# Kernel tuning notes

Measured on AMD Instinct MI355X. Metric: run time of the kernel, lower is better.

## Reference

```python
import jax, jax.numpy as jnp
import numpy as np

N, F, F_, H = 8192, 1024, 64, 4
LEAKY_ALPHA = 0.2
MASK_VAL = -1e10


def setup_inputs() -> dict:
    key = jax.random.key(0)
    k1, k2, k3, k4 = jax.random.split(key, 4)
    X = jax.random.normal(k1, (N, F), dtype=jnp.float32)
    # sparse-ish binary adjacency with self loops (A = A + I in the source script)
    A = (jax.random.uniform(k2, (N, N)) < 0.004).astype(jnp.float32)
    A = jnp.clip(A + jnp.eye(N, dtype=jnp.float32), 0.0, 1.0)
    W = jax.random.normal(k3, (H, F, F_), dtype=jnp.float32) * (1.0 / np.sqrt(F))
    attn_a = jax.random.normal(k4, (H, 2 * F_, 1), dtype=jnp.float32) * (1.0 / np.sqrt(2 * F_))
    bias = jnp.zeros((H, F_), dtype=jnp.float32)
    return {"X": X, "A": A, "W": W, "attn_a": attn_a, "bias": bias}


def reference(X, A, W, attn_a, bias):
    # features per head: [H, N, F_]
    feats = jnp.einsum('nf,hfk->hnk', X, W)
    # concat-score trick: [f_i, f_j] @ a == f_i @ a[:F_] + f_j @ a[F_:]
    a_self = attn_a[:, :F_, 0]   # [H, F_]
    a_neigh = attn_a[:, F_:, 0]  # [H, F_]
    s_self = jnp.einsum('hnk,hk->hn', feats, a_self)   # [H, N]
    s_neigh = jnp.einsum('hnk,hk->hn', feats, a_neigh)  # [H, N]
    scores = s_self[:, :, None] + s_neigh[:, None, :]   # [H, N, N]
    scores = jnp.where(scores > 0, scores, LEAKY_ALPHA * scores)  # LeakyReLU(0.2)
    scores = scores + MASK_VAL * (1.0 - A)[None]
    attn = jax.nn.softmax(scores, axis=-1)              # [H, N, N]
    # aggregate (dropout is identity at inference)
    out = jnp.einsum('hij,hjk->hik', attn, feats) + bias[:, None, :]  # [H, N, F_]
    out = jnp.transpose(out, (1, 0, 2)).reshape(X.shape[0], H * F_)   # concat heads
    return jax.nn.relu(out)
```

## Files before the change

### kernel.cpp

```cpp
#include <hip/hip_runtime.h>
#include <hip/hip_bf16.h>
#include <stdint.h>

#define NN 8192
#define FF 1024
#define FD 64
#define NH 4
#define CC 256
#define MAXE 192

typedef __attribute__((ext_vector_type(8))) short short8;
typedef __attribute__((ext_vector_type(4))) float f32x4;

__device__ __forceinline__ short bf16_rne(float f) {
    union { float f; uint32_t u; } v; v.f = f;
    uint32_t r = (v.u + 0x7FFFu + ((v.u >> 16) & 1u)) >> 16;
    return (short)(r & 0xFFFFu);
}
__device__ __forceinline__ float bf2f(short s) {
    union { uint32_t u; float f; } v; v.u = ((uint32_t)(uint16_t)s) << 16;
    return v.f;
}

__global__ __launch_bounds__(256) void wt_kernel(const float* __restrict__ W,
                                                 short* __restrict__ Wt) {
    int gid = blockIdx.x * 256 + threadIdx.x;
    int k = gid & 1023;
    int n = (gid >> 10) & 63;
    int h = gid >> 16;
    Wt[gid] = bf16_rne(W[(h << 16) + k * 64 + n]);
}

__global__ __launch_bounds__(256) void mega_kernel(const float* __restrict__ X,
                                                   const short* __restrict__ Wt,
                                                   const float* __restrict__ attn_a,
                                                   const float* __restrict__ A,
                                                   short* __restrict__ featb,
                                                   float* __restrict__ s_self4,
                                                   float* __restrict__ s_neigh4,
                                                   int* __restrict__ nbr,
                                                   int* __restrict__ cnt) {
    __shared__ short Xs[64 * 40];
    __shared__ short Ws[64 * 40];
    const int b = blockIdx.x;
    const int t = threadIdx.x;

    if (b < 512) {
        const int h  = b & 3;
        const int m0 = (b >> 2) * 64;
        const int wave = t >> 6, lane = t & 63;
        const int q = lane >> 4, nl = lane & 15;
        const int srow = t >> 2, sk8 = (t & 3) * 8;

        f32x4 acc0 = {0.f,0.f,0.f,0.f}, acc1 = {0.f,0.f,0.f,0.f};
        f32x4 acc2 = {0.f,0.f,0.f,0.f}, acc3 = {0.f,0.f,0.f,0.f};

        const float* Xp = X + (size_t)(m0 + srow) * FF + sk8;
        const short* Wp = Wt + (size_t)(h * 64 + srow) * FF + sk8;

        for (int k0 = 0; k0 < FF; k0 += 32) {
            float4 x0 = *(const float4*)(Xp + k0);
            float4 x1 = *(const float4*)(Xp + k0 + 4);
            short8 wv = *(const short8*)(Wp + k0);
            short8 xv;
            xv[0] = bf16_rne(x0.x); xv[1] = bf16_rne(x0.y);
            xv[2] = bf16_rne(x0.z); xv[3] = bf16_rne(x0.w);
            xv[4] = bf16_rne(x1.x); xv[5] = bf16_rne(x1.y);
            xv[6] = bf16_rne(x1.z); xv[7] = bf16_rne(x1.w);
            *(short8*)(&Xs[srow * 40 + sk8]) = xv;
            *(short8*)(&Ws[srow * 40 + sk8]) = wv;
            __syncthreads();
            short8 a  = *(const short8*)(&Xs[(wave * 16 + nl) * 40 + q * 8]);
            short8 b0 = *(const short8*)(&Ws[( 0 + nl) * 40 + q * 8]);
            short8 b1 = *(const short8*)(&Ws[(16 + nl) * 40 + q * 8]);
            short8 b2 = *(const short8*)(&Ws[(32 + nl) * 40 + q * 8]);
            short8 b3 = *(const short8*)(&Ws[(48 + nl) * 40 + q * 8]);
            acc0 = __builtin_amdgcn_mfma_f32_16x16x32_bf16(a, b0, acc0, 0, 0, 0);
            acc1 = __builtin_amdgcn_mfma_f32_16x16x32_bf16(a, b1, acc1, 0, 0, 0);
            acc2 = __builtin_amdgcn_mfma_f32_16x16x32_bf16(a, b2, acc2, 0, 0, 0);
            acc3 = __builtin_amdgcn_mfma_f32_16x16x32_bf16(a, b3, acc3, 0, 0, 0);
            __syncthreads();
        }
        const int row = m0 + wave * 16 + q * 4;
        const int colbase = h * 64 + nl;
        for (int r = 0; r < 4; ++r) {
            short* fr = featb + (size_t)(row + r) * CC + colbase;
            fr[ 0] = bf16_rne(acc0[r]);
            fr[16] = bf16_rne(acc1[r]);
            fr[32] = bf16_rne(acc2[r]);
            fr[48] = bf16_rne(acc3[r]);
        }
        const float A0 = attn_a[h * 128 + nl],      A1 = attn_a[h * 128 + nl + 16];
        const float A2 = attn_a[h * 128 + nl + 32], A3 = attn_a[h * 128 + nl + 48];
        const float B0 = attn_a[h * 128 + 64 + nl],      B1 = attn_a[h * 128 + 64 + nl + 16];
        const float B2 = attn_a[h * 128 + 64 + nl + 32], B3 = attn_a[h * 128 + 64 + nl + 48];
        for (int r = 0; r < 4; ++r) {
            float ps = acc0[r] * A0 + acc1[r] * A1 + acc2[r] * A2 + acc3[r] * A3;
            float pn = acc0[r] * B0 + acc1[r] * B1 + acc2[r] * B2 + acc3[r] * B3;
            for (int off = 1; off < 16; off <<= 1) {
                ps += __shfl_xor(ps, off);
                pn += __shfl_xor(pn, off);
            }
            if (nl == 0) {
                s_self4 [(row + r) * 4 + h] = ps;
                s_neigh4[(row + r) * 4 + h] = pn;
            }
        }
    } else {
        int* idx = (int*)Xs;
        int* c   = (int*)Ws;
        const int row = b - 512;
        if (t == 0) *c = 0;
        __syncthreads();
        const f32x4* A4 = (const f32x4*)(A + (size_t)row * NN);
        for (int r = 0; r < 8; ++r) {
            int c4 = r * 256 + t;
            f32x4 v = __builtin_nontemporal_load(&A4[c4]);
            if (v.x > 0.5f) { int p = atomicAdd(c, 1); if (p < MAXE) idx[p] = c4 * 4 + 0; }
            if (v.y > 0.5f) { int p = atomicAdd(c, 1); if (p < MAXE) idx[p] = c4 * 4 + 1; }
            if (v.z > 0.5f) { int p = atomicAdd(c, 1); if (p < MAXE) idx[p] = c4 * 4 + 2; }
            if (v.w > 0.5f) { int p = atomicAdd(c, 1); if (p < MAXE) idx[p] = c4 * 4 + 3; }
        }
        __syncthreads();
        int n = min(*c, MAXE);
        if (t < n) nbr[row * MAXE + t] = idx[t];
        if (t == 0) cnt[row] = n;
    }
}

__global__ __launch_bounds__(256) void smax_kernel(const int* __restrict__ nbr,
                                                   const int* __restrict__ cnt,
                                                   const short* __restrict__ featb,
                                                   const float* __restrict__ s_self4,
                                                   const float* __restrict__ s_neigh4,
                                                   const float* __restrict__ bias,
                                                   float* __restrict__ out) {
    __shared__ int js[MAXE];
    __shared__ float scs[NH][MAXE];
    const int row = blockIdx.x;
    const int t = threadIdx.x;
    const int h = t >> 6, lane = t & 63;
    const int n = cnt[row];
    if (t < n) js[t] = nbr[row * MAXE + t];
    __syncthreads();

    const f32x4 ss = *(const f32x4*)(s_self4 + row * 4);
    if (t < n) {
        f32x4 sn = *(const f32x4*)(s_neigh4 + js[t] * 4);
        #pragma unroll
        for (int hh = 0; hh < NH; ++hh) {
            float s = ss[hh] + sn[hh];
            scs[hh][t] = s > 0.f ? s : 0.2f * s;
        }
    }
    __syncthreads();

    float m = -1e30f;
    #pragma unroll
    for (int i = 0; i < 3; ++i) {
        int e = lane + 64 * i;
        if (e < n) m = fmaxf(m, scs[h][e]);
    }
    for (int off = 1; off < 64; off <<= 1) m = fmaxf(m, __shfl_xor(m, off));
    float dsum = 0.f;
    #pragma unroll
    for (int i = 0; i < 3; ++i) {
        int e = lane + 64 * i;
        if (e < n) {
            float p = __expf(scs[h][e] - m);
            scs[h][e] = p;
            dsum += p;
        }
    }
    for (int off = 1; off < 64; off <<= 1) dsum += __shfl_xor(dsum, off);

    const int sub = lane >> 3;
    const int l8  = lane & 7;
    const short* fb = featb + h * 64 + l8 * 8;
    f32x4 accA = {0.f,0.f,0.f,0.f}, accB = {0.f,0.f,0.f,0.f};
    for (int e = sub; e < n; e += 8) {
        int j = js[e];
        float p = scs[h][e];
        short8 f = *(const short8*)(fb + (size_t)j * CC);
        accA[0] = fmaf(p, bf2f(f[0]), accA[0]);
        accA[1] = fmaf(p, bf2f(f[1]), accA[1]);
        accA[2] = fmaf(p, bf2f(f[2]), accA[2]);
        accA[3] = fmaf(p, bf2f(f[3]), accA[3]);
        accB[0] = fmaf(p, bf2f(f[4]), accB[0]);
        accB[1] = fmaf(p, bf2f(f[5]), accB[1]);
        accB[2] = fmaf(p, bf2f(f[6]), accB[2]);
        accB[3] = fmaf(p, bf2f(f[7]), accB[3]);
    }
    #pragma unroll
    for (int k = 0; k < 4; ++k) {
        accA[k] += __shfl_xor(accA[k], 8);
        accA[k] += __shfl_xor(accA[k], 16);
        accA[k] += __shfl_xor(accA[k], 32);
        accB[k] += __shfl_xor(accB[k], 8);
        accB[k] += __shfl_xor(accB[k], 16);
        accB[k] += __shfl_xor(accB[k], 32);
    }
    if (sub == 0) {
        float rd = 1.0f / dsum;
        const float* bp = bias + h * 64 + l8 * 8;
        f32x4 oA, oB;
        #pragma unroll
        for (int k = 0; k < 4; ++k) {
            oA[k] = fmaxf(accA[k] * rd + bp[k],     0.f);
            oB[k] = fmaxf(accB[k] * rd + bp[k + 4], 0.f);
        }
        float* op = out + (size_t)row * CC + h * 64 + l8 * 8;
        *(f32x4*)op       = oA;
        *(f32x4*)(op + 4) = oB;
    }
}

extern "C" void kernel_launch(void* const* d_in, const int* in_sizes, int n_in,
                              void* d_out, int out_size, void* d_ws, size_t ws_size,
                              hipStream_t stream) {
    const float* X      = (const float*)d_in[0];
    const float* A      = (const float*)d_in[1];
    const float* W      = (const float*)d_in[2];
    const float* attn_a = (const float*)d_in[3];
    const float* bias   = (const float*)d_in[4];
    float* out = (float*)d_out;

    char* ws = (char*)d_ws;
    short* featb    = (short*)ws;
    float* s_self4  = (float*)(ws + 4194304);
    float* s_neigh4 = (float*)(ws + 4325376);
    short* Wt       = (short*)(ws + 4456448);
    int*   nbr      = (int*)  (ws + 4980736);
    int*   cnt      = (int*)  (ws + 11272192);

    wt_kernel  <<<1024, 256, 0, stream>>>(W, Wt);
    mega_kernel<<<512 + NN, 256, 0, stream>>>(X, Wt, attn_a, A,
                                              featb, s_self4, s_neigh4, nbr, cnt);
    smax_kernel<<<NN, 256, 0, stream>>>(nbr, cnt, featb, s_self4, s_neigh4, bias, out);
}
```

Baseline: 406.6 us.

## Fuse all stages into one cooperative persistent kernel with grid syncs

Merges the W transpose, the adjacency compaction, the feature GEMM and the sparse softmax aggregation into a single cooperative kernel of 1024 persistent blocks, separated by grid-wide syncs. It is meant to remove the launch overhead and tail gaps between three kernels. In exchange, the GEMM phase now runs on only 512 of the 1024 blocks while the rest sit idle, the A-scan no longer overlaps with the GEMM, and the grid syncs add cost. The design also depends on all 1024 blocks being co-resident.

New measurement: 694.0 us. 1.71x slower.

```diff
diff --git a/kernel.cpp b/kernel.cpp
--- a/kernel.cpp
+++ b/kernel.cpp
@@ -1,13 +1,15 @@
 #include <hip/hip_runtime.h>
-#include <hip/hip_bf16.h>
+#include <hip/hip_cooperative_groups.h>
 #include <stdint.h>
+
+namespace cg = cooperative_groups;
 
 #define NN 8192
 #define FF 1024
-#define FD 64
 #define NH 4
 #define CC 256
 #define MAXE 192
+#define GRID 1024
 
 typedef __attribute__((ext_vector_type(8))) short short8;
 typedef __attribute__((ext_vector_type(4))) float f32x4;
@@ -22,30 +24,55 @@
     return v.f;
 }
 
-__global__ __launch_bounds__(256) void wt_kernel(const float* __restrict__ W,
-                                                 short* __restrict__ Wt) {
-    int gid = blockIdx.x * 256 + threadIdx.x;
-    int k = gid & 1023;
-    int n = (gid >> 10) & 63;
-    int h = gid >> 16;
-    Wt[gid] = bf16_rne(W[(h << 16) + k * 64 + n]);
-}
-
-__global__ __launch_bounds__(256) void mega_kernel(const float* __restrict__ X,
-                                                   const short* __restrict__ Wt,
-                                                   const float* __restrict__ attn_a,
-                                                   const float* __restrict__ A,
-                                                   short* __restrict__ featb,
-                                                   float* __restrict__ s_self4,
-                                                   float* __restrict__ s_neigh4,
-                                                   int* __restrict__ nbr,
-                                                   int* __restrict__ cnt) {
-    __shared__ short Xs[64 * 40];
-    __shared__ short Ws[64 * 40];
+__global__ __launch_bounds__(256, 4) void fused_kernel(
+    const float* __restrict__ X, const float* __restrict__ A,
+    const float* __restrict__ W, const float* __restrict__ attn_a,
+    const float* __restrict__ bias,
+    short* __restrict__ Wt, short* __restrict__ featb,
+    float* __restrict__ s_self4, float* __restrict__ s_neigh4,
+    int* __restrict__ nbr, int* __restrict__ cnt,
+    float* __restrict__ out)
+{
+    cg::grid_group grid = cg::this_grid();
+    __shared__ short lds[2 * 64 * 40];
+    __shared__ int c;
     const int b = blockIdx.x;
     const int t = threadIdx.x;
 
+    {
+        int gid = b * 256 + t;
+        int k = gid & 1023, n = (gid >> 10) & 63, h = gid >> 16;
+        Wt[gid] = bf16_rne(W[(h << 16) + k * 64 + n]);
+    }
+
+    {
+        int* idx = (int*)lds;
+        for (int row = b; row < NN; row += GRID) {
+            if (t == 0) c = 0;
+            __syncthreads();
+            const f32x4* A4 = (const f32x4*)(A + (size_t)row * NN);
+            #pragma unroll
+            for (int r = 0; r < 8; ++r) {
+                int c4 = r * 256 + t;
+                f32x4 v = __builtin_nontemporal_load(&A4[c4]);
+                if (v.x > 0.5f) { int p = atomicAdd(&c, 1); if (p < MAXE) idx[p] = c4 * 4 + 0; }
+                if (v.y > 0.5f) { int p = atomicAdd(&c, 1); if (p < MAXE) idx[p] = c4 * 4 + 1; }
+                if (v.z > 0.5f) { int p = atomicAdd(&c, 1); if (p < MAXE) idx[p] = c4 * 4 + 2; }
+                if (v.w > 0.5f) { int p = atomicAdd(&c, 1); if (p < MAXE) idx[p] = c4 * 4 + 3; }
+            }
+            __syncthreads();
+            int n = min(c, MAXE);
+            if (t < n) nbr[row * MAXE + t] = idx[t];
+            if (t == 0) cnt[row] = n;
+            __syncthreads();
+        }
+    }
+
+    grid.sync();
+
     if (b < 512) {
+        short* Xs = lds;
+        short* Ws = lds + 64 * 40;
         const int h  = b & 3;
         const int m0 = (b >> 2) * 64;
         const int wave = t >> 6, lane = t & 63;
@@ -106,112 +133,92 @@
                 s_neigh4[(row + r) * 4 + h] = pn;
             }
         }
-    } else {
-        int* idx = (int*)Xs;
-        int* c   = (int*)Ws;
-        const int row = b - 512;
-        if (t == 0) *c = 0;
-        __syncthreads();
-        const f32x4* A4 = (const f32x4*)(A + (size_t)row * NN);
-        for (int r = 0; r < 8; ++r) {
-            int c4 = r * 256 + t;
-            f32x4 v = __builtin_nontemporal_load(&A4[c4]);
-            if (v.x > 0.5f) { int p = atomicAdd(c, 1); if (p < MAXE) idx[p] = c4 * 4 + 0; }
-            if (v.y > 0.5f) { int p = atomicAdd(c, 1); if (p < MAXE) idx[p] = c4 * 4 + 1; }
-            if (v.z > 0.5f) { int p = atomicAdd(c, 1); if (p < MAXE) idx[p] = c4 * 4 + 2; }
-            if (v.w > 0.5f) { int p = atomicAdd(c, 1); if (p < MAXE) idx[p] = c4 * 4 + 3; }
-        }
-        __syncthreads();
-        int n = min(*c, MAXE);
-        if (t < n) nbr[row * MAXE + t] = idx[t];
-        if (t == 0) cnt[row] = n;
-    }
-}
-
-__global__ __launch_bounds__(256) void smax_kernel(const int* __restrict__ nbr,
-                                                   const int* __restrict__ cnt,
-                                                   const short* __restrict__ featb,
-                                                   const float* __restrict__ s_self4,
-                                                   const float* __restrict__ s_neigh4,
-                                                   const float* __restrict__ bias,
-                                                   float* __restrict__ out) {
-    __shared__ int js[MAXE];
-    __shared__ float scs[NH][MAXE];
-    const int row = blockIdx.x;
-    const int t = threadIdx.x;
-    const int h = t >> 6, lane = t & 63;
-    const int n = cnt[row];
-    if (t < n) js[t] = nbr[row * MAXE + t];
-    __syncthreads();
-
-    const f32x4 ss = *(const f32x4*)(s_self4 + row * 4);
-    if (t < n) {
-        f32x4 sn = *(const f32x4*)(s_neigh4 + js[t] * 4);
-        #pragma unroll
-        for (int hh = 0; hh < NH; ++hh) {
-            float s = ss[hh] + sn[hh];
-            scs[hh][t] = s > 0.f ? s : 0.2f * s;
-        }
-    }
-    __syncthreads();
-
-    float m = -1e30f;
-    #pragma unroll
-    for (int i = 0; i < 3; ++i) {
-        int e = lane + 64 * i;
-        if (e < n) m = fmaxf(m, scs[h][e]);
-    }
-    for (int off = 1; off < 64; off <<= 1) m = fmaxf(m, __shfl_xor(m, off));
-    float dsum = 0.f;
-    #pragma unroll
-    for (int i = 0; i < 3; ++i) {
-        int e = lane + 64 * i;
-        if (e < n) {
-            float p = __expf(scs[h][e] - m);
-            scs[h][e] = p;
-            dsum += p;
-        }
-    }
-    for (int off = 1; off < 64; off <<= 1) dsum += __shfl_xor(dsum, off);
-
-    const int sub = lane >> 3;
-    const int l8  = lane & 7;
-    const short* fb = featb + h * 64 + l8 * 8;
-    f32x4 accA = {0.f,0.f,0.f,0.f}, accB = {0.f,0.f,0.f,0.f};
-    for (int e = sub; e < n; e += 8) {
-        int j = js[e];
-        float p = scs[h][e];
-        short8 f = *(const short8*)(fb + (size_t)j * CC);
-        accA[0] = fmaf(p, bf2f(f[0]), accA[0]);
-        accA[1] = fmaf(p, bf2f(f[1]), accA[1]);
-        accA[2] = fmaf(p, bf2f(f[2]), accA[2]);
-        accA[3] = fmaf(p, bf2f(f[3]), accA[3]);
-        accB[0] = fmaf(p, bf2f(f[4]), accB[0]);
-        accB[1] = fmaf(p, bf2f(f[5]), accB[1]);
-        accB[2] = fmaf(p, bf2f(f[6]), accB[2]);
-        accB[3] = fmaf(p, bf2f(f[7]), accB[3]);
-    }
-    #pragma unroll
-    for (int k = 0; k < 4; ++k) {
-        accA[k] += __shfl_xor(accA[k], 8);
-        accA[k] += __shfl_xor(accA[k], 16);
-        accA[k] += __shfl_xor(accA[k], 32);
-        accB[k] += __shfl_xor(accB[k], 8);
-        accB[k] += __shfl_xor(accB[k], 16);
-        accB[k] += __shfl_xor(accB[k], 32);
-    }
-    if (sub == 0) {
-        float rd = 1.0f / dsum;
-        const float* bp = bias + h * 64 + l8 * 8;
-        f32x4 oA, oB;
-        #pragma unroll
-        for (int k = 0; k < 4; ++k) {
-            oA[k] = fmaxf(accA[k] * rd + bp[k],     0.f);
-            oB[k] = fmaxf(accB[k] * rd + bp[k + 4], 0.f);
-        }
-        float* op = out + (size_t)row * CC + h * 64 + l8 * 8;
-        *(f32x4*)op       = oA;
-        *(f32x4*)(op + 4) = oB;
+    }
+
+    grid.sync();
+
+    {
+        int*   js  = (int*)lds;
+        float* scs = (float*)(lds + MAXE * 2);
+        const int h = t >> 6, lane = t & 63;
+
+        for (int row = b; row < NN; row += GRID) {
+            __syncthreads();
+            const int n = cnt[row];
+            if (t < n) js[t] = nbr[row * MAXE + t];
+            __syncthreads();
+
+            const f32x4 ss = *(const f32x4*)(s_self4 + row * 4);
+            if (t < n) {
+                f32x4 sn = *(const f32x4*)(s_neigh4 + js[t] * 4);
+                #pragma unroll
+                for (int hh = 0; hh < NH; ++hh) {
+                    float s = ss[hh] + sn[hh];
+                    (scs + hh * MAXE)[t] = s > 0.f ? s : 0.2f * s;
+                }
+            }
+            __syncthreads();
+
+            float* sch = scs + h * MAXE;
+            float m = -1e30f;
+            #pragma unroll
+            for (int i = 0; i < 3; ++i) {
+                int e = lane + 64 * i;
+                if (e < n) m = fmaxf(m, sch[e]);
+            }
+            for (int off = 1; off < 64; off <<= 1) m = fmaxf(m, __shfl_xor(m, off));
+            float dsum = 0.f;
+            #pragma unroll
+            for (int i = 0; i < 3; ++i) {
+                int e = lane + 64 * i;
+                if (e < n) {
+                    float p = __expf(sch[e] - m);
+                    sch[e] = p;
+                    dsum += p;
+                }
+            }
+            for (int off = 1; off < 64; off <<= 1) dsum += __shfl_xor(dsum, off);
+
+            const int sub = lane >> 3;
+            const int l8  = lane & 7;
+            const short* fb = featb + h * 64 + l8 * 8;
+            f32x4 accA = {0.f,0.f,0.f,0.f}, accB = {0.f,0.f,0.f,0.f};
+            for (int e = sub; e < n; e += 8) {
+                int j = js[e];
+                float p = sch[e];
+                short8 f = *(const short8*)(fb + (size_t)j * CC);
+                accA[0] = fmaf(p, bf2f(f[0]), accA[0]);
+                accA[1] = fmaf(p, bf2f(f[1]), accA[1]);
+                accA[2] = fmaf(p, bf2f(f[2]), accA[2]);
+                accA[3] = fmaf(p, bf2f(f[3]), accA[3]);
+                accB[0] = fmaf(p, bf2f(f[4]), accB[0]);
+                accB[1] = fmaf(p, bf2f(f[5]), accB[1]);
+                accB[2] = fmaf(p, bf2f(f[6]), accB[2]);
+                accB[3] = fmaf(p, bf2f(f[7]), accB[3]);
+            }
+            #pragma unroll
+            for (int k = 0; k < 4; ++k) {
+                accA[k] += __shfl_xor(accA[k], 8);
+                accA[k] += __shfl_xor(accA[k], 16);
+                accA[k] += __shfl_xor(accA[k], 32);
+                accB[k] += __shfl_xor(accB[k], 8);
+                accB[k] += __shfl_xor(accB[k], 16);
+                accB[k] += __shfl_xor(accB[k], 32);
+            }
+            if (sub == 0) {
+                float rd = 1.0f / dsum;
+                const float* bp = bias + h * 64 + l8 * 8;
+                f32x4 oA, oB;
+                #pragma unroll
+                for (int k = 0; k < 4; ++k) {
+                    oA[k] = fmaxf(accA[k] * rd + bp[k],     0.f);
+                    oB[k] = fmaxf(accB[k] * rd + bp[k + 4], 0.f);
+                }
+                float* op = out + (size_t)row * CC + h * 64 + l8 * 8;
+                *(f32x4*)op       = oA;
+                *(f32x4*)(op + 4) = oB;
+            }
+        }
     }
 }
 
@@ -233,8 +240,9 @@
     int*   nbr      = (int*)  (ws + 4980736);
     int*   cnt      = (int*)  (ws + 11272192);
 
-    wt_kernel  <<<1024, 256, 0, stream>>>(W, Wt);
-    mega_kernel<<<512 + NN, 256, 0, stream>>>(X, Wt, attn_a, A,
-                                              featb, s_self4, s_neigh4, nbr, cnt);
-    smax_kernel<<<NN, 256, 0, stream>>>(nbr, cnt, featb, s_self4, s_neigh4, bias, out);
-}
+    void* args[] = { (void*)&X, (void*)&A, (void*)&W, (void*)&attn_a, (void*)&bias,
+                     (void*)&Wt, (void*)&featb, (void*)&s_self4, (void*)&s_neigh4,
+                     (void*)&nbr, (void*)&cnt, (void*)&out };
+    hipLaunchCooperativeKernel((void*)fused_kernel, dim3(GRID), dim3(256),
+                               args, 0, stream);
+}
```

## Fuse adjacency scan into softmax kernel, separate GEMM into its own launch

Applied to the files above, without the earlier changes.

Moves the per-row adjacency scan out of the combined GEMM/scan kernel and into the softmax-aggregation kernel, so neighbor indices stay in shared memory instead of being written to and reread from global nbr/cnt buffers. The GEMM becomes its own 512-block launch. This removes a global round trip for the neighbor lists. In exchange, the scan no longer overlaps with the GEMM blocks: the GEMM now runs alone on only 512 blocks before the A-streaming pass starts.

After: 407.9 us. No clear change (+0.3%).

```diff
diff --git a/kernel.cpp b/kernel.cpp
--- a/kernel.cpp
+++ b/kernel.cpp
@@ -1,10 +1,8 @@
 #include <hip/hip_runtime.h>
-#include <hip/hip_bf16.h>
 #include <stdint.h>
 
 #define NN 8192
 #define FF 1024
-#define FD 64
 #define NH 4
 #define CC 256
 #define MAXE 192
@@ -31,118 +29,105 @@
     Wt[gid] = bf16_rne(W[(h << 16) + k * 64 + n]);
 }
 
-__global__ __launch_bounds__(256) void mega_kernel(const float* __restrict__ X,
+__global__ __launch_bounds__(256) void gemm_kernel(const float* __restrict__ X,
                                                    const short* __restrict__ Wt,
                                                    const float* __restrict__ attn_a,
-                                                   const float* __restrict__ A,
                                                    short* __restrict__ featb,
                                                    float* __restrict__ s_self4,
-                                                   float* __restrict__ s_neigh4,
-                                                   int* __restrict__ nbr,
-                                                   int* __restrict__ cnt) {
+                                                   float* __restrict__ s_neigh4) {
     __shared__ short Xs[64 * 40];
     __shared__ short Ws[64 * 40];
     const int b = blockIdx.x;
-    const int t = threadIdx.x;
-
-    if (b < 512) {
-        const int h  = b & 3;
-        const int m0 = (b >> 2) * 64;
-        const int wave = t >> 6, lane = t & 63;
-        const int q = lane >> 4, nl = lane & 15;
-        const int srow = t >> 2, sk8 = (t & 3) * 8;
-
-        f32x4 acc0 = {0.f,0.f,0.f,0.f}, acc1 = {0.f,0.f,0.f,0.f};
-        f32x4 acc2 = {0.f,0.f,0.f,0.f}, acc3 = {0.f,0.f,0.f,0.f};
-
-        const float* Xp = X + (size_t)(m0 + srow) * FF + sk8;
-        const short* Wp = Wt + (size_t)(h * 64 + srow) * FF + sk8;
-
-        for (int k0 = 0; k0 < FF; k0 += 32) {
-            float4 x0 = *(const float4*)(Xp + k0);
-            float4 x1 = *(const float4*)(Xp + k0 + 4);
-            short8 wv = *(const short8*)(Wp + k0);
-            short8 xv;
-            xv[0] = bf16_rne(x0.x); xv[1] = bf16_rne(x0.y);
-            xv[2] = bf16_rne(x0.z); xv[3] = bf16_rne(x0.w);
-            xv[4] = bf16_rne(x1.x); xv[5] = bf16_rne(x1.y);
-            xv[6] = bf16_rne(x1.z); xv[7] = bf16_rne(x1.w);
-            *(short8*)(&Xs[srow * 40 + sk8]) = xv;
-            *(short8*)(&Ws[srow * 40 + sk8]) = wv;
-            __syncthreads();
-            short8 a  = *(const short8*)(&Xs[(wave * 16 + nl) * 40 + q * 8]);
-            short8 b0 = *(const short8*)(&Ws[( 0 + nl) * 40 + q * 8]);
-            short8 b1 = *(const short8*)(&Ws[(16 + nl) * 40 + q * 8]);
-            short8 b2 = *(const short8*)(&Ws[(32 + nl) * 40 + q * 8]);
-            short8 b3 = *(const short8*)(&Ws[(48 + nl) * 40 + q * 8]);
-            acc0 = __builtin_amdgcn_mfma_f32_16x16x32_bf16(a, b0, acc0, 0, 0, 0);
-            acc1 = __builtin_amdgcn_mfma_f32_16x16x32_bf16(a, b1, acc1, 0, 0, 0);
-            acc2 = __builtin_amdgcn_mfma_f32_16x16x32_bf16(a, b2, acc2, 0, 0, 0);
-            acc3 = __builtin_amdgcn_mfma_f32_16x16x32_bf16(a, b3, acc3, 0, 0, 0);
-            __syncthreads();
-        }
-        const int row = m0 + wave * 16 + q * 4;
-        const int colbase = h * 64 + nl;
-        for (int r = 0; r < 4; ++r) {
-            short* fr = featb + (size_t)(row + r) * CC + colbase;
-            fr[ 0] = bf16_rne(acc0[r]);
-            fr[16] = bf16_rne(acc1[r]);
-            fr[32] = bf16_rne(acc2[r]);
-            fr[48] = bf16_rne(acc3[r]);
-        }
-        const float A0 = attn_a[h * 128 + nl],      A1 = attn_a[h * 128 + nl + 16];
-        const float A2 = attn_a[h * 128 + nl + 32], A3 = attn_a[h * 128 + nl + 48];
-        const float B0 = attn_a[h * 128 + 64 + nl],      B1 = attn_a[h * 128 + 64 + nl + 16];
-        const float B2 = attn_a[h * 128 + 64 + nl + 32], B3 = attn_a[h * 128 + 64 + nl + 48];
-        for (int r = 0; r < 4; ++r) {
-            float ps = acc0[r] * A0 + acc1[r] * A1 + acc2[r] * A2 + acc3[r] * A3;
-            float pn = acc0[r] * B0 + acc1[r] * B1 + acc2[r] * B2 + acc3[r] * B3;
-            for (int off = 1; off < 16; off <<= 1) {
-                ps += __shfl_xor(ps, off);
-                pn += __shfl_xor(pn, off);
-            }
-            if (nl == 0) {
-                s_self4 [(row + r) * 4 + h] = ps;
-                s_neigh4[(row + r) * 4 + h] = pn;
-            }
-        }
-    } else {
-        int* idx = (int*)Xs;
-        int* c   = (int*)Ws;
-        const int row = b - 512;
-        if (t == 0) *c = 0;
+    const int h  = b & 3;
+    const int m0 = (b >> 2) * 64;
+    const int t  = threadIdx.x;
+    const int wave = t >> 6, lane = t & 63;
+    const int q = lane >> 4, nl = lane & 15;
+    const int srow = t >> 2, sk8 = (t & 3) * 8;
+
+    f32x4 acc0 = {0.f,0.f,0.f,0.f}, acc1 = {0.f,0.f,0.f,0.f};
+    f32x4 acc2 = {0.f,0.f,0.f,0.f}, acc3 = {0.f,0.f,0.f,0.f};
+
+    const float* Xp = X + (size_t)(m0 + srow) * FF + sk8;
+    const short* Wp = Wt + (size_t)(h * 64 + srow) * FF + sk8;
+
+    for (int k0 = 0; k0 < FF; k0 += 32) {
+        float4 x0 = *(const float4*)(Xp + k0);
+        float4 x1 = *(const float4*)(Xp + k0 + 4);
+        short8 wv = *(const short8*)(Wp + k0);
+        short8 xv;
+        xv[0] = bf16_rne(x0.x); xv[1] = bf16_rne(x0.y);
+        xv[2] = bf16_rne(x0.z); xv[3] = bf16_rne(x0.w);
+        xv[4] = bf16_rne(x1.x); xv[5] = bf16_rne(x1.y);
+        xv[6] = bf16_rne(x1.z); xv[7] = bf16_rne(x1.w);
+        *(short8*)(&Xs[srow * 40 + sk8]) = xv;
+        *(short8*)(&Ws[srow * 40 + sk8]) = wv;
         __syncthreads();
-        const f32x4* A4 = (const f32x4*)(A + (size_t)row * NN);
-        for (int r = 0; r < 8; ++r) {
-            int c4 = r * 256 + t;
-            f32x4 v = __builtin_nontemporal_load(&A4[c4]);
-            if (v.x > 0.5f) { int p = atomicAdd(c, 1); if (p < MAXE) idx[p] = c4 * 4 + 0; }
-            if (v.y > 0.5f) { int p = atomicAdd(c, 1); if (p < MAXE) idx[p] = c4 * 4 + 1; }
-            if (v.z > 0.5f) { int p = atomicAdd(c, 1); if (p < MAXE) idx[p] = c4 * 4 + 2; }
-            if (v.w > 0.5f) { int p = atomicAdd(c, 1); if (p < MAXE) idx[p] = c4 * 4 + 3; }
-        }
+        short8 a  = *(const short8*)(&Xs[(wave * 16 + nl) * 40 + q * 8]);
+        short8 b0 = *(const short8*)(&Ws[( 0 + nl) * 40 + q * 8]);
+        short8 b1 = *(const short8*)(&Ws[(16 + nl) * 40 + q * 8]);
+        short8 b2 = *(const short8*)(&Ws[(32 + nl) * 40 + q * 8]);
+        short8 b3 = *(const short8*)(&Ws[(48 + nl) * 40 + q * 8]);
+        acc0 = __builtin_amdgcn_mfma_f32_16x16x32_bf16(a, b0, acc0, 0, 0, 0);
+        acc1 = __builtin_amdgcn_mfma_f32_16x16x32_bf16(a, b1, acc1, 0, 0, 0);
+        acc2 = __builtin_amdgcn_mfma_f32_16x16x32_bf16(a, b2, acc2, 0, 0, 0);
+        acc3 = __builtin_amdgcn_mfma_f32_16x16x32_bf16(a, b3, acc3, 0, 0, 0);
         __syncthreads();
-        int n = min(*c, MAXE);
-        if (t < n) nbr[row * MAXE + t] = idx[t];
-        if (t == 0) cnt[row] = n;
-    }
-}
-
-__global__ __launch_bounds__(256) void smax_kernel(const int* __restrict__ nbr,
-                                                   const int* __restrict__ cnt,
-                                                   const short* __restrict__ featb,
-                                                   const float* __restrict__ s_self4,
-                                                   const float* __restrict__ s_neigh4,
-                                                   const float* __restrict__ bias,
-                                                   float* __restrict__ out) {
+    }
+    const int row = m0 + wave * 16 + q * 4;
+    const int colbase = h * 64 + nl;
+    for (int r = 0; r < 4; ++r) {
+        short* fr = featb + (size_t)(row + r) * CC + colbase;
+        fr[ 0] = bf16_rne(acc0[r]);
+        fr[16] = bf16_rne(acc1[r]);
+        fr[32] = bf16_rne(acc2[r]);
+        fr[48] = bf16_rne(acc3[r]);
+    }
+    const float A0 = attn_a[h * 128 + nl],      A1 = attn_a[h * 128 + nl + 16];
+    const float A2 = attn_a[h * 128 + nl + 32], A3 = attn_a[h * 128 + nl + 48];
+    const float B0 = attn_a[h * 128 + 64 + nl],      B1 = attn_a[h * 128 + 64 + nl + 16];
+    const float B2 = attn_a[h * 128 + 64 + nl + 32], B3 = attn_a[h * 128 + 64 + nl + 48];
+    for (int r = 0; r < 4; ++r) {
+        float ps = acc0[r] * A0 + acc1[r] * A1 + acc2[r] * A2 + acc3[r] * A3;
+        float pn = acc0[r] * B0 + acc1[r] * B1 + acc2[r] * B2 + acc3[r] * B3;
+        for (int off = 1; off < 16; off <<= 1) {
+            ps += __shfl_xor(ps, off);
+            pn += __shfl_xor(pn, off);
+        }
+        if (nl == 0) {
+            s_self4 [(row + r) * 4 + h] = ps;
+            s_neigh4[(row + r) * 4 + h] = pn;
+        }
+    }
+}
+
+__global__ __launch_bounds__(256) void scanmax_kernel(const float* __restrict__ A,
+                                                      const short* __restrict__ featb,
+                                                      const float* __restrict__ s_self4,
+                                                      const float* __restrict__ s_neigh4,
+                                                      const float* __restrict__ bias,
+                                                      float* __restrict__ out) {
     __shared__ int js[MAXE];
     __shared__ float scs[NH][MAXE];
+    __shared__ int c;
     const int row = blockIdx.x;
     const int t = threadIdx.x;
+    if (t == 0) c = 0;
+    __syncthreads();
+
+    const f32x4* A4 = (const f32x4*)(A + (size_t)row * NN);
+    #pragma unroll
+    for (int r = 0; r < 8; ++r) {
+        int c4 = r * 256 + t;
+        f32x4 v = __builtin_nontemporal_load(&A4[c4]);
+        if (v.x > 0.5f) { int p = atomicAdd(&c, 1); if (p < MAXE) js[p] = c4 * 4 + 0; }
+        if (v.y > 0.5f) { int p = atomicAdd(&c, 1); if (p < MAXE) js[p] = c4 * 4 + 1; }
+        if (v.z > 0.5f) { int p = atomicAdd(&c, 1); if (p < MAXE) js[p] = c4 * 4 + 2; }
+        if (v.w > 0.5f) { int p = atomicAdd(&c, 1); if (p < MAXE) js[p] = c4 * 4 + 3; }
+    }
+    __syncthreads();
+    const int n = min(c, MAXE);
     const int h = t >> 6, lane = t & 63;
-    const int n = cnt[row];
-    if (t < n) js[t] = nbr[row * MAXE + t];
-    __syncthreads();
 
     const f32x4 ss = *(const f32x4*)(s_self4 + row * 4);
     if (t < n) {
@@ -230,11 +215,8 @@
     float* s_self4  = (float*)(ws + 4194304);
     float* s_neigh4 = (float*)(ws + 4325376);
     short* Wt       = (short*)(ws + 4456448);
-    int*   nbr      = (int*)  (ws + 4980736);
-    int*   cnt      = (int*)  (ws + 11272192);
-
-    wt_kernel  <<<1024, 256, 0, stream>>>(W, Wt);
-    mega_kernel<<<512 + NN, 256, 0, stream>>>(X, Wt, attn_a, A,
-                                              featb, s_self4, s_neigh4, nbr, cnt);
-    smax_kernel<<<NN, 256, 0, stream>>>(nbr, cnt, featb, s_self4, s_neigh4, bias, out);
-}
+
+    wt_kernel     <<<1024, 256, 0, stream>>>(W, Wt);
+    gemm_kernel   <<<512,  256, 0, stream>>>(X, Wt, attn_a, featb, s_self4, s_neigh4);
+    scanmax_kernel<<<NN,   256, 0, stream>>>(A, featb, s_self4, s_neigh4, bias, out);
+}
```
